# Performance work log

Hardware: AMD Instinct MI355X
Metric: run time of the kernel (lower is better)

Reference implementation:

```python
import jax, jax.numpy as jnp
import numpy as np

N = 10000
E = 320000
IN_CH = 256
OUT4 = 256  # 4 * out_channels, out_channels = 64


def setup_inputs() -> dict:
    key = jax.random.key(0)
    k1, k2, k3 = jax.random.split(key, 3)
    x = jax.random.normal(k1, (N, IN_CH), dtype=jnp.float32)
    edge_index = jax.random.randint(k2, (2, E), 0, N, dtype=jnp.int64)
    stdv = 1.0 / np.sqrt(64.0)  # 1/sqrt(out_channels), as in __init__
    weight = jax.random.uniform(k3, (IN_CH, OUT4), dtype=jnp.float32,
                                minval=-stdv, maxval=stdv)
    return {"x": x, "weight": weight, "edge_index": edge_index}


def reference(x, weight, edge_index):
    n = x.shape[0]
    idx = jnp.arange(n)
    # dense adjacency with self-loops (duplicates/edges just set to 1)
    adj = jnp.zeros((n, n), dtype=x.dtype)
    adj = adj.at[idx, idx].set(1.0)
    adj = adj.at[edge_index[0], edge_index[1]].set(1.0)
    # symmetric degree normalization D^-1/2 A D^-1/2
    deg = jnp.sum(adj, axis=1)  # >= 1 due to self-loops
    d_inv_sqrt = jax.lax.rsqrt(deg)
    norm_adj = adj * d_inv_sqrt[:, None] * d_inv_sqrt[None, :]
    # aggregate then project: (A_norm @ x) @ W
    return jnp.matmul(jnp.matmul(norm_adj, x), weight)
```

## Files before the change

### kernel.cpp

```cpp
#include <hip/hip_runtime.h>


#define CH 256
#define ELLW 96

typedef __attribute__((ext_vector_type(8))) short short8;
typedef __attribute__((ext_vector_type(4))) float f32x4;

__device__ inline unsigned short f2b(float f) {
    unsigned x = __builtin_bit_cast(unsigned, f);
    x = (x + 0x7fffu + ((x >> 16) & 1u)) >> 16;
    return (unsigned short)x;
}
__device__ inline float b2f(unsigned short u) {
    unsigned v = ((unsigned)u) << 16;
    return __builtin_bit_cast(float, v);
}

__global__ void prep_kernel(int* cnt, int n, const float* __restrict__ w,
                            unsigned short* __restrict__ wt) {
    int t = blockIdx.x * blockDim.x + threadIdx.x;
    if (t < n) {
        cnt[t] = 0;
    } else if (t < n + CH * CH) {
        int idx = t - n;
        int k = idx >> 8, nn = idx & 255;
        wt[nn * CH + k] = f2b(w[idx]);
    }
}

__global__ __launch_bounds__(256) void fillgemm_kernel(
    const int* __restrict__ ei, int e_cnt, int* cnt, int* __restrict__ col_ell,
    const float* __restrict__ x, const unsigned short* __restrict__ wt,
    unsigned short* __restrict__ zb, int n, int fillb) {
    if ((int)blockIdx.x < fillb) {
        int e = blockIdx.x * blockDim.x + threadIdx.x;
        if (e < e_cnt) {
            int r = ei[e];
            int c = ei[e_cnt + e];
            int pos = atomicAdd(&cnt[r], 1);
            if (pos < ELLW) col_ell[(size_t)r * ELLW + pos] = c;
        }
        return;
    }
    const int blk = blockIdx.x - fillb;
    const int tid = threadIdx.x;
    const int lane = tid & 63;
    const int wv = tid >> 6;
    const int m0 = blk * 16;
    const int n0 = wv * 64;
    const int rsel = lane & 15;
    const int kbase = (lane >> 4) * 8;

    const float* xrow = x + (size_t)(m0 + rsel) * CH + kbase;
    const unsigned short* b0p = wt + (size_t)(n0 + rsel) * CH + kbase;
    const unsigned short* b1p = b0p + 16 * CH;
    const unsigned short* b2p = b0p + 32 * CH;
    const unsigned short* b3p = b0p + 48 * CH;

    f32x4 acc0 = {0.f, 0.f, 0.f, 0.f};
    f32x4 acc1 = acc0, acc2 = acc0, acc3 = acc0;

#pragma unroll
    for (int kc = 0; kc < 8; ++kc) {
        const float4* p = (const float4*)(xrow + kc * 32);
        float4 u = p[0], v = p[1];
        short8 a;
        a[0] = (short)f2b(u.x); a[1] = (short)f2b(u.y);
        a[2] = (short)f2b(u.z); a[3] = (short)f2b(u.w);
        a[4] = (short)f2b(v.x); a[5] = (short)f2b(v.y);
        a[6] = (short)f2b(v.z); a[7] = (short)f2b(v.w);
        short8 b0 = *(const short8*)(b0p + kc * 32);
        short8 b1 = *(const short8*)(b1p + kc * 32);
        short8 b2 = *(const short8*)(b2p + kc * 32);
        short8 b3 = *(const short8*)(b3p + kc * 32);
        acc0 = __builtin_amdgcn_mfma_f32_16x16x32_bf16(a, b0, acc0, 0, 0, 0);
        acc1 = __builtin_amdgcn_mfma_f32_16x16x32_bf16(a, b1, acc1, 0, 0, 0);
        acc2 = __builtin_amdgcn_mfma_f32_16x16x32_bf16(a, b2, acc2, 0, 0, 0);
        acc3 = __builtin_amdgcn_mfma_f32_16x16x32_bf16(a, b3, acc3, 0, 0, 0);
    }

    const int r0 = (lane >> 4) * 4;
    const int slice = n0 >> 7;
    const int nn0 = n0 & 127;
#pragma unroll
    for (int j = 0; j < 4; ++j) {
        unsigned short* zr = zb + ((size_t)slice * n + (m0 + r0 + j)) * 128 + nn0 + rsel;
        zr[0]  = f2b(acc0[j]);
        zr[16] = f2b(acc1[j]);
        zr[32] = f2b(acc2[j]);
        zr[48] = f2b(acc3[j]);
    }
}

__global__ __launch_bounds__(256) void dedup_kernel(
    int* cnt, int* __restrict__ col_ell, float* __restrict__ dinv, int n) {
    __shared__ int sh[4][ELLW];
    const int wv = threadIdx.x >> 6, lane = threadIdx.x & 63;
    const int r = blockIdx.x * 4 + wv;

    int m = 0;
    if (r < n) { m = cnt[r]; if (m > ELLW) m = ELLW; }
    for (int e = lane; e < m; e += 64) sh[wv][e] = col_ell[(size_t)r * ELLW + e];
    __syncthreads();

    if (r < n) {
        const int e0 = lane, e1 = 64 + lane;
        int c0 = (e0 < m) ? sh[wv][e0] : -1;
        int c1 = (e1 < m) ? sh[wv][e1] : -1;
        bool dup0 = (c0 == r), dup1 = (c1 == r);
        for (int k = 0; k < m; ++k) {
            int ck = sh[wv][k];
            dup0 |= (k < e0) && (ck == c0);
            dup1 |= (k < e1) && (ck == c1);
        }
        unsigned long long b0 = __ballot((e0 < m) && !dup0);
        unsigned long long b1 = __ballot((e1 < m) && !dup1);
        unsigned long long lt = (1ull << lane) - 1ull;
        int n0 = __popcll(b0);
        int mm = n0 + __popcll(b1);
        if (mm != m) {
            if ((e0 < m) && !dup0)
                col_ell[(size_t)r * ELLW + __popcll(b0 & lt)] = c0;
            if ((e1 < m) && !dup1)
                col_ell[(size_t)r * ELLW + n0 + __popcll(b1 & lt)] = c1;
            if (lane == 0) cnt[r] = mm;
        }
        if (lane == 0) dinv[r] = rsqrtf((float)(mm + 1));
    }
}

__global__ __launch_bounds__(256) void gather_kernel(
    const int* __restrict__ cnt, const int* __restrict__ col_ell,
    const float* __restrict__ dinv,
    const unsigned short* __restrict__ zb, float* __restrict__ out, int n) {
    const int b = blockIdx.x;
    const int slice = b & 1;
    const int wv = threadIdx.x >> 6;
    const int wid = (b >> 1) * 4 + wv;
    if (wid >= n) return;
    const int lane = threadIdx.x & 63;
    const int g = lane >> 4;
    const int chb = (lane & 15) * 8;
    int m = cnt[wid]; if (m > ELLW) m = ELLW;
    const int* cl = col_ell + (size_t)wid * ELLW;
    const unsigned short* zs = zb + (size_t)slice * n * 128 + chb;
    const float dr = dinv[wid];

    float acc[8];
    if (g == 0) {
        short8 s = *(const short8*)(zs + (size_t)wid * 128);
#pragma unroll
        for (int q = 0; q < 8; ++q) acc[q] = dr * b2f((unsigned short)s[q]);
    } else {
#pragma unroll
        for (int q = 0; q < 8; ++q) acc[q] = 0.f;
    }

    int idx = g;
    for (; idx + 12 < m; idx += 16) {
        int c0 = cl[idx], c1 = cl[idx + 4], c2 = cl[idx + 8], c3 = cl[idx + 12];
        float d0 = dinv[c0], d1 = dinv[c1], d2 = dinv[c2], d3 = dinv[c3];
        short8 v0 = *(const short8*)(zs + (size_t)c0 * 128);
        short8 v1 = *(const short8*)(zs + (size_t)c1 * 128);
        short8 v2 = *(const short8*)(zs + (size_t)c2 * 128);
        short8 v3 = *(const short8*)(zs + (size_t)c3 * 128);
#pragma unroll
        for (int q = 0; q < 8; ++q)
            acc[q] += d0 * b2f((unsigned short)v0[q]) + d1 * b2f((unsigned short)v1[q])
                    + d2 * b2f((unsigned short)v2[q]) + d3 * b2f((unsigned short)v3[q]);
    }
    for (; idx < m; idx += 4) {
        int c = cl[idx];
        float dc = dinv[c];
        short8 v = *(const short8*)(zs + (size_t)c * 128);
#pragma unroll
        for (int q = 0; q < 8; ++q) acc[q] += dc * b2f((unsigned short)v[q]);
    }

#pragma unroll
    for (int q = 0; q < 8; ++q) acc[q] += __shfl_xor(acc[q], 16);
#pragma unroll
    for (int q = 0; q < 8; ++q) acc[q] += __shfl_xor(acc[q], 32);

    if (g == 0) {
        float* dst = out + (size_t)wid * CH + slice * 128 + chb;
        float4 o0, o1;
        o0.x = acc[0] * dr; o0.y = acc[1] * dr; o0.z = acc[2] * dr; o0.w = acc[3] * dr;
        o1.x = acc[4] * dr; o1.y = acc[5] * dr; o1.z = acc[6] * dr; o1.w = acc[7] * dr;
        *(float4*)dst = o0;
        *(float4*)(dst + 4) = o1;
    }
}

extern "C" void kernel_launch(void* const* d_in, const int* in_sizes, int n_in,
                              void* d_out, int out_size, void* d_ws, size_t ws_size,
                              hipStream_t stream) {
    const float* x = (const float*)d_in[0];
    const float* w = (const float*)d_in[1];
    const int* ei = (const int*)d_in[2];
    float* out = (float*)d_out;

    const int n = in_sizes[0] / CH;
    const int e_cnt = in_sizes[2] / 2;

    char* ws = (char*)d_ws;
    size_t off = 0;
    unsigned short* zb = (unsigned short*)(ws + off); off += (size_t)n * CH * 2;
    unsigned short* wt = (unsigned short*)(ws + off); off += (size_t)CH * CH * 2;
    int* cnt = (int*)(ws + off);      off += (size_t)n * 4;
    float* dinv = (float*)(ws + off); off += (size_t)n * 4;
    int* col_ell = (int*)(ws + off);  off += (size_t)n * ELLW * 4;

    prep_kernel<<<(n + CH * CH + 255) / 256, 256, 0, stream>>>(cnt, n, w, wt);

    const int fillb = (e_cnt + 255) / 256;
    fillgemm_kernel<<<fillb + n / 16, 256, 0, stream>>>(ei, e_cnt, cnt, col_ell,
                                                        x, wt, zb, n, fillb);

    dedup_kernel<<<(n + 3) / 4, 256, 0, stream>>>(cnt, col_ell, dinv, n);

    gather_kernel<<<2 * ((n + 3) / 4), 256, 0, stream>>>(cnt, col_ell, dinv, zb, out, n);
}
```

Before: 77.12 us.

## Replace global atomic ELL fill with two-pass block-local bucketing and merge

Edge scattering now bins edges per block into 32-row buckets using shared-memory atomics, writing packed (row,col) into a per-block region with a fixed capacity. A merge kernel per bucket gathers all blocks' entries into shared memory, then deduplicates and writes the ELL rows and degrees. This removes global atomics on cnt and the cnt zeroing. The cost is a large region buffer and serial per-thread loops in merge over 1250 blocks. It also relies on 16-bit row/col packing and a per-bucket capacity of 12 that could drop edges.

```diff
diff --git a/kernel.cpp b/kernel.cpp
--- a/kernel.cpp
+++ b/kernel.cpp
@@ -3,6 +3,9 @@
 
 #define CH 256
 #define ELLW 96
+#define CAP 12
+#define RPBK 32
+#define NBMAX 320
 
 typedef __attribute__((ext_vector_type(8))) short short8;
 typedef __attribute__((ext_vector_type(4))) float f32x4;
@@ -17,30 +20,36 @@
     return __builtin_bit_cast(float, v);
 }
 
-__global__ void prep_kernel(int* cnt, int n, const float* __restrict__ w,
+__global__ void prep_kernel(const float* __restrict__ w,
                             unsigned short* __restrict__ wt) {
-    int t = blockIdx.x * blockDim.x + threadIdx.x;
-    if (t < n) {
-        cnt[t] = 0;
-    } else if (t < n + CH * CH) {
-        int idx = t - n;
+    int idx = blockIdx.x * blockDim.x + threadIdx.x;
+    if (idx < CH * CH) {
         int k = idx >> 8, nn = idx & 255;
         wt[nn * CH + k] = f2b(w[idx]);
     }
 }
 
-__global__ __launch_bounds__(256) void fillgemm_kernel(
-    const int* __restrict__ ei, int e_cnt, int* cnt, int* __restrict__ col_ell,
+__global__ __launch_bounds__(256) void partgemm_kernel(
+    const int* __restrict__ ei, int e_cnt, int nb,
+    unsigned* __restrict__ region, int* __restrict__ counts,
     const float* __restrict__ x, const unsigned short* __restrict__ wt,
     unsigned short* __restrict__ zb, int n, int fillb) {
+    __shared__ int hist[NBMAX];
     if ((int)blockIdx.x < fillb) {
-        int e = blockIdx.x * blockDim.x + threadIdx.x;
+        const int b = blockIdx.x;
+        for (int i = threadIdx.x; i < nb; i += 256) hist[i] = 0;
+        __syncthreads();
+        int e = b * 256 + threadIdx.x;
         if (e < e_cnt) {
             int r = ei[e];
             int c = ei[e_cnt + e];
-            int pos = atomicAdd(&cnt[r], 1);
-            if (pos < ELLW) col_ell[(size_t)r * ELLW + pos] = c;
-        }
+            int k = r >> 5;
+            int p = atomicAdd(&hist[k], 1);
+            if (p < CAP)
+                region[((size_t)b * nb + k) * CAP + p] = ((unsigned)r << 16) | (unsigned)c;
+        }
+        __syncthreads();
+        for (int i = threadIdx.x; i < nb; i += 256) counts[(size_t)b * nb + i] = hist[i];
         return;
     }
     const int blk = blockIdx.x - fillb;
@@ -93,40 +102,57 @@
     }
 }
 
-__global__ __launch_bounds__(256) void dedup_kernel(
-    int* cnt, int* __restrict__ col_ell, float* __restrict__ dinv, int n) {
-    __shared__ int sh[4][ELLW];
+__global__ __launch_bounds__(256) void merge_kernel(
+    const unsigned* __restrict__ region, const int* __restrict__ counts,
+    int nb, int fillb, int* __restrict__ cnt, int* __restrict__ col_ell,
+    float* __restrict__ dinv, int n) {
+    __shared__ int lcol[RPBK][ELLW];
+    __shared__ int lcnt[RPBK];
+    const int k = blockIdx.x;
+    for (int i = threadIdx.x; i < RPBK; i += 256) lcnt[i] = 0;
+    __syncthreads();
+
+    for (int b = threadIdx.x; b < fillb; b += 256) {
+        int m = counts[(size_t)b * nb + k];
+        if (m > CAP) m = CAP;
+        const unsigned* rp = region + ((size_t)b * nb + k) * CAP;
+        for (int j = 0; j < m; ++j) {
+            unsigned u = rp[j];
+            int ri = (int)(u >> 16) & (RPBK - 1);
+            int c = (int)(u & 0xFFFFu);
+            int p = atomicAdd(&lcnt[ri], 1);
+            if (p < ELLW) lcol[ri][p] = c;
+        }
+    }
+    __syncthreads();
+
     const int wv = threadIdx.x >> 6, lane = threadIdx.x & 63;
-    const int r = blockIdx.x * 4 + wv;
-
-    int m = 0;
-    if (r < n) { m = cnt[r]; if (m > ELLW) m = ELLW; }
-    for (int e = lane; e < m; e += 64) sh[wv][e] = col_ell[(size_t)r * ELLW + e];
-    __syncthreads();
-
-    if (r < n) {
+    const unsigned long long lt = (1ull << lane) - 1ull;
+    for (int ri = wv; ri < RPBK; ri += 4) {
+        const int r = k * RPBK + ri;
+        if (r >= n) break;
+        int m = lcnt[ri]; if (m > ELLW) m = ELLW;
         const int e0 = lane, e1 = 64 + lane;
-        int c0 = (e0 < m) ? sh[wv][e0] : -1;
-        int c1 = (e1 < m) ? sh[wv][e1] : -1;
+        int c0 = (e0 < m) ? lcol[ri][e0] : -1;
+        int c1 = (e1 < m) ? lcol[ri][e1] : -1;
         bool dup0 = (c0 == r), dup1 = (c1 == r);
-        for (int k = 0; k < m; ++k) {
-            int ck = sh[wv][k];
-            dup0 |= (k < e0) && (ck == c0);
-            dup1 |= (k < e1) && (ck == c1);
+        for (int j = 0; j < m; ++j) {
+            int cj = lcol[ri][j];
+            dup0 |= (j < e0) && (cj == c0);
+            dup1 |= (j < e1) && (cj == c1);
         }
         unsigned long long b0 = __ballot((e0 < m) && !dup0);
         unsigned long long b1 = __ballot((e1 < m) && !dup1);
-        unsigned long long lt = (1ull << lane) - 1ull;
         int n0 = __popcll(b0);
         int mm = n0 + __popcll(b1);
-        if (mm != m) {
-            if ((e0 < m) && !dup0)
-                col_ell[(size_t)r * ELLW + __popcll(b0 & lt)] = c0;
-            if ((e1 < m) && !dup1)
-                col_ell[(size_t)r * ELLW + n0 + __popcll(b1 & lt)] = c1;
-            if (lane == 0) cnt[r] = mm;
-        }
-        if (lane == 0) dinv[r] = rsqrtf((float)(mm + 1));
+        if ((e0 < m) && !dup0)
+            col_ell[(size_t)r * ELLW + __popcll(b0 & lt)] = c0;
+        if ((e1 < m) && !dup1)
+            col_ell[(size_t)r * ELLW + n0 + __popcll(b1 & lt)] = c1;
+        if (lane == 0) {
+            cnt[r] = mm;
+            dinv[r] = rsqrtf((float)(mm + 1));
+        }
     }
 }
 
@@ -203,6 +229,8 @@
 
     const int n = in_sizes[0] / CH;
     const int e_cnt = in_sizes[2] / 2;
+    const int nb = (n + RPBK - 1) / RPBK;
+    const int fillb = (e_cnt + 255) / 256;
 
     char* ws = (char*)d_ws;
     size_t off = 0;
@@ -211,14 +239,15 @@
     int* cnt = (int*)(ws + off);      off += (size_t)n * 4;
     float* dinv = (float*)(ws + off); off += (size_t)n * 4;
     int* col_ell = (int*)(ws + off);  off += (size_t)n * ELLW * 4;
-
-    prep_kernel<<<(n + CH * CH + 255) / 256, 256, 0, stream>>>(cnt, n, w, wt);
-
-    const int fillb = (e_cnt + 255) / 256;
-    fillgemm_kernel<<<fillb + n / 16, 256, 0, stream>>>(ei, e_cnt, cnt, col_ell,
+    unsigned* region = (unsigned*)(ws + off); off += (size_t)fillb * nb * CAP * 4;
+    int* counts = (int*)(ws + off);   off += (size_t)fillb * nb * 4;
+
+    prep_kernel<<<(CH * CH + 255) / 256, 256, 0, stream>>>(w, wt);
+
+    partgemm_kernel<<<fillb + n / 16, 256, 0, stream>>>(ei, e_cnt, nb, region, counts,
                                                         x, wt, zb, n, fillb);
 
-    dedup_kernel<<<(n + 3) / 4, 256, 0, stream>>>(cnt, col_ell, dinv, n);
+    merge_kernel<<<nb, 256, 0, stream>>>(region, counts, nb, fillb, cnt, col_ell, dinv, n);
 
     gather_kernel<<<2 * ((n + 3) / 4), 256, 0, stream>>>(cnt, col_ell, dinv, zb, out, n);
 }
```

After: 88.95 us. 1.15x slower.
